# Kernel optimization log

Hardware: AMD Instinct MI355X
Metric: run time of the kernel (lower is better)

Reference implementation:

```python
import jax, jax.numpy as jnp
import numpy as np

LEAKY_SLOPE = 0.2   # LeakyReLU alpha from __init__
MASK_VAL = -9.0e15  # same sentinel as torch reference


def setup_inputs() -> dict:
    key = jax.random.key(0)
    k1, k2, k3 = jax.random.split(key, 3)
    B, N, D = 512, 64, 128
    hidden = jax.random.normal(k1, (B, N, D), dtype=jnp.float32)
    adj = jax.random.randint(k2, (B, N, N), 0, 5)  # edge types 0..4
    a = jax.random.normal(k3, (4, D), dtype=jnp.float32) * 0.1  # stacked a_0..a_3
    return {"hidden": hidden, "adj": adj, "a": a}


def reference(hidden, adj, a):
    # e_k[b,i,j] = leakyrelu( sum_d hidden[b,i,d]*hidden[b,j,d]*a[k,d] )
    # Never materializes the [B,N,N,D] tensor: contract (hidden * a_k) @ hidden^T.
    e = jnp.einsum('kd,bid,bjd->kbij', a, hidden, hidden)  # [4,B,N,N]
    e = jnp.where(e >= 0, e, LEAKY_SLOPE * e)
    mask = jnp.full(e.shape[1:], MASK_VAL, dtype=e.dtype)
    alpha = jnp.where(adj == 1, e[0], mask)
    alpha = jnp.where(adj == 2, e[1], alpha)
    alpha = jnp.where(adj == 3, e[2], alpha)
    alpha = jnp.where(adj == 4, e[3], alpha)
    alpha = jax.nn.softmax(alpha, axis=-1)          # [B,N,N]
    return jnp.matmul(alpha, hidden)                # [B,N,D]
```

## Files before the change

### kernel.cpp

```cpp
#include <hip/hip_runtime.h>
#include <hip/hip_bf16.h>


#define NB 512
#define NN 64
#define ND 128
#define HS 136
#define AS 72

typedef __bf16 bf16x8 __attribute__((ext_vector_type(8)));
typedef __bf16 bf16x4 __attribute__((ext_vector_type(4)));
typedef float  f32x4  __attribute__((ext_vector_type(4)));

__global__ __launch_bounds__(256)
void gat_kernel(const float* __restrict__ hidden,
                const int*   __restrict__ adj,
                const float* __restrict__ a,
                float*       __restrict__ out)
{
    __shared__ __bf16 h_lds[NN * HS];
    __shared__ __bf16 h_tr[8 * NN * 16];
    __shared__ __bf16 al_lds[NN * AS];
    __shared__ float  a_lds[4 * ND];

    const int t = threadIdx.x;
    const int l = t & 63;
    const int w = t >> 6;
    const int b = blockIdx.x;
    const int g  = l >> 4;
    const int g8 = g << 3;
    const int i0 = w * 16 + (g << 2);

    const int* adjb = adj + (size_t)b * NN * NN;
    int adjv[4][4];
    #pragma unroll
    for (int ct = 0; ct < 4; ++ct)
        #pragma unroll
        for (int r = 0; r < 4; ++r)
            adjv[ct][r] = adjb[(i0 + r) * NN + ct * 16 + (l & 15)];

    const float4* hin = (const float4*)(hidden + (size_t)b * NN * ND);
    #pragma unroll
    for (int it = 0; it < 8; ++it) {
        int row = ((l >> 2) & 15) | ((it >> 1) << 4);
        int f4  = (l & 3) | (w << 2) | ((it & 1) << 4);
        float4 v = hin[row * 32 + f4];
        bf16x4 pk = { (__bf16)v.x, (__bf16)v.y, (__bf16)v.z, (__bf16)v.w };
        int c4 = f4 << 2;
        *(bf16x4*)&h_lds[row * HS + c4] = pk;
        *(bf16x4*)&h_tr[((c4 >> 4) << 10) + (row << 4) + (c4 & 15)] = pk;
    }
    a_lds[t]       = a[t];
    a_lds[t + 256] = a[t + 256];
    __syncthreads();

    const int irow = w * 16 + (l & 15);
    f32x4 acc[4][4];
    #pragma unroll
    for (int ct = 0; ct < 4; ++ct)
        #pragma unroll
        for (int k = 0; k < 4; ++k)
            acc[ct][k] = (f32x4){0.f, 0.f, 0.f, 0.f};

    #pragma unroll
    for (int kk = 0; kk < 4; ++kk) {
        int d0 = kk * 32 + g8;
        bf16x8 hf = *(const bf16x8*)&h_lds[irow * HS + d0];
        float hff[8];
        #pragma unroll
        for (int e = 0; e < 8; ++e) hff[e] = (float)hf[e];
        bf16x8 hk[4];
        #pragma unroll
        for (int k = 0; k < 4; ++k) {
            float4 alo = *(const float4*)&a_lds[k * ND + d0];
            float4 ahi = *(const float4*)&a_lds[k * ND + d0 + 4];
            bf16x8 r;
            r[0] = (__bf16)(hff[0] * alo.x); r[1] = (__bf16)(hff[1] * alo.y);
            r[2] = (__bf16)(hff[2] * alo.z); r[3] = (__bf16)(hff[3] * alo.w);
            r[4] = (__bf16)(hff[4] * ahi.x); r[5] = (__bf16)(hff[5] * ahi.y);
            r[6] = (__bf16)(hff[6] * ahi.z); r[7] = (__bf16)(hff[7] * ahi.w);
            hk[k] = r;
        }
        bf16x8 bfr[4];
        #pragma unroll
        for (int ct = 0; ct < 4; ++ct)
            bfr[ct] = *(const bf16x8*)&h_lds[(ct * 16 + (l & 15)) * HS + d0];
        #pragma unroll
        for (int ct = 0; ct < 4; ++ct)
            #pragma unroll
            for (int k = 0; k < 4; ++k)
                acc[ct][k] = __builtin_amdgcn_mfma_f32_16x16x32_bf16(hk[k], bfr[ct], acc[ct][k], 0, 0, 0);
    }

    float sel[4][4];
    #pragma unroll
    for (int ct = 0; ct < 4; ++ct)
        #pragma unroll
        for (int r = 0; r < 4; ++r) {
            float e0 = fmaxf(acc[ct][0][r], 0.2f * acc[ct][0][r]);
            float e1 = fmaxf(acc[ct][1][r], 0.2f * acc[ct][1][r]);
            float e2 = fmaxf(acc[ct][2][r], 0.2f * acc[ct][2][r]);
            float e3 = fmaxf(acc[ct][3][r], 0.2f * acc[ct][3][r]);
            int av = adjv[ct][r];
            sel[ct][r] = av == 1 ? e0 : av == 2 ? e1 : av == 3 ? e2 : av == 4 ? e3 : -9.0e15f;
        }

    float inv[4];
    #pragma unroll
    for (int r = 0; r < 4; ++r) {
        float m = fmaxf(fmaxf(sel[0][r], sel[1][r]), fmaxf(sel[2][r], sel[3][r]));
        m = fmaxf(m, __shfl_xor(m, 1));
        m = fmaxf(m, __shfl_xor(m, 2));
        m = fmaxf(m, __shfl_xor(m, 4));
        m = fmaxf(m, __shfl_xor(m, 8));
        float p0 = __expf(sel[0][r] - m);
        float p1 = __expf(sel[1][r] - m);
        float p2 = __expf(sel[2][r] - m);
        float p3 = __expf(sel[3][r] - m);
        float s = p0 + p1 + p2 + p3;
        s += __shfl_xor(s, 1);
        s += __shfl_xor(s, 2);
        s += __shfl_xor(s, 4);
        s += __shfl_xor(s, 8);
        inv[r] = 1.0f / s;
        int i = i0 + r;
        al_lds[i * AS +  0 + (l & 15)] = (__bf16)p0;
        al_lds[i * AS + 16 + (l & 15)] = (__bf16)p1;
        al_lds[i * AS + 32 + (l & 15)] = (__bf16)p2;
        al_lds[i * AS + 48 + (l & 15)] = (__bf16)p3;
    }

    const int ia = w * 16 + (l & 15);
    bf16x8 aA0 = *(const bf16x8*)&al_lds[ia * AS + g8];
    bf16x8 aA1 = *(const bf16x8*)&al_lds[ia * AS + 32 + g8];
    float* outb = out + (size_t)b * NN * ND;
    unsigned trb = (unsigned)(unsigned long long)(&h_tr[0])
                 + (unsigned)(((l & 15) << 3) + (g << 8));
    #pragma unroll
    for (int dt = 0; dt < 8; ++dt) {
        unsigned ab = trb + dt * 2048;
        bf16x4 r0, r1, r2, r3;
        asm volatile("ds_read_b64_tr_b16 %0, %1"             : "=v"(r0) : "v"(ab));
        asm volatile("ds_read_b64_tr_b16 %0, %1 offset:128"  : "=v"(r1) : "v"(ab));
        asm volatile("ds_read_b64_tr_b16 %0, %1 offset:1024" : "=v"(r2) : "v"(ab));
        asm volatile("ds_read_b64_tr_b16 %0, %1 offset:1152" : "=v"(r3) : "v"(ab));
        asm volatile("s_waitcnt lgkmcnt(0)" ::: "memory");
        __builtin_amdgcn_sched_barrier(0);
        bf16x8 B0 = __builtin_shufflevector(r0, r1, 0, 1, 2, 3, 4, 5, 6, 7);
        bf16x8 B1 = __builtin_shufflevector(r2, r3, 0, 1, 2, 3, 4, 5, 6, 7);
        f32x4 o = {0.f, 0.f, 0.f, 0.f};
        o = __builtin_amdgcn_mfma_f32_16x16x32_bf16(aA0, B0, o, 0, 0, 0);
        o = __builtin_amdgcn_mfma_f32_16x16x32_bf16(aA1, B1, o, 0, 0, 0);
        int dr = dt * 16 + (l & 15);
        #pragma unroll
        for (int r = 0; r < 4; ++r)
            outb[(i0 + r) * ND + dr] = o[r] * inv[r];
    }
}

extern "C" void kernel_launch(void* const* d_in, const int* in_sizes, int n_in,
                              void* d_out, int out_size, void* d_ws, size_t ws_size,
                              hipStream_t stream) {
    const float* hidden = (const float*)d_in[0];
    const int*   adj    = (const int*)d_in[1];
    const float* a      = (const float*)d_in[2];
    float*       out    = (float*)d_out;
    gat_kernel<<<NB, 256, 0, stream>>>(hidden, adj, a, out);
}
```

Baseline: 16.62 us.

## Stage adjacency in LDS and swap MFMA operands for vectorized output stores

Adjacency is now loaded with coalesced int4 global reads into a padded LDS tile instead of 16 scattered scalar global loads per thread. The softmax normalization is folded into the bf16 probabilities before the second matmul. The MFMA operand order is swapped so each lane holds four consecutive output columns of one row, which allows float4 stores instead of scalar stores. The cost is extra LDS space (about 16KB), which may lower occupancy, plus scalar LDS writes for the adjacency tile and slight precision loss from normalizing before rounding to bf16.

New measurement: 17.12 us. 3.0% more time.

```diff
diff --git a/kernel.cpp b/kernel.cpp
--- a/kernel.cpp
+++ b/kernel.cpp
@@ -7,6 +7,7 @@
 #define ND 128
 #define HS 136
 #define AS 72
+#define AJS 65
 
 typedef __bf16 bf16x8 __attribute__((ext_vector_type(8)));
 typedef __bf16 bf16x4 __attribute__((ext_vector_type(4)));
@@ -22,6 +23,7 @@
     __shared__ __bf16 h_tr[8 * NN * 16];
     __shared__ __bf16 al_lds[NN * AS];
     __shared__ float  a_lds[4 * ND];
+    __shared__ int    adj_lds[NN * AJS];
 
     const int t = threadIdx.x;
     const int l = t & 63;
@@ -30,14 +32,6 @@
     const int g  = l >> 4;
     const int g8 = g << 3;
     const int i0 = w * 16 + (g << 2);
-
-    const int* adjb = adj + (size_t)b * NN * NN;
-    int adjv[4][4];
-    #pragma unroll
-    for (int ct = 0; ct < 4; ++ct)
-        #pragma unroll
-        for (int r = 0; r < 4; ++r)
-            adjv[ct][r] = adjb[(i0 + r) * NN + ct * 16 + (l & 15)];
 
     const float4* hin = (const float4*)(hidden + (size_t)b * NN * ND);
     #pragma unroll
@@ -49,6 +43,16 @@
         int c4 = f4 << 2;
         *(bf16x4*)&h_lds[row * HS + c4] = pk;
         *(bf16x4*)&h_tr[((c4 >> 4) << 10) + (row << 4) + (c4 & 15)] = pk;
+    }
+    const int4* adjin = (const int4*)(adj + (size_t)b * NN * NN);
+    #pragma unroll
+    for (int it = 0; it < 4; ++it) {
+        int idx = it * 256 + t;
+        int4 v = adjin[idx];
+        int ri = idx >> 4;
+        int c4 = (idx & 15) << 2;
+        int* p = &adj_lds[ri * AJS + c4];
+        p[0] = v.x; p[1] = v.y; p[2] = v.z; p[3] = v.w;
     }
     a_lds[t]       = a[t];
     a_lds[t + 256] = a[t + 256];
@@ -97,15 +101,14 @@
     for (int ct = 0; ct < 4; ++ct)
         #pragma unroll
         for (int r = 0; r < 4; ++r) {
+            int av = adj_lds[(i0 + r) * AJS + ct * 16 + (l & 15)];
             float e0 = fmaxf(acc[ct][0][r], 0.2f * acc[ct][0][r]);
             float e1 = fmaxf(acc[ct][1][r], 0.2f * acc[ct][1][r]);
             float e2 = fmaxf(acc[ct][2][r], 0.2f * acc[ct][2][r]);
             float e3 = fmaxf(acc[ct][3][r], 0.2f * acc[ct][3][r]);
-            int av = adjv[ct][r];
             sel[ct][r] = av == 1 ? e0 : av == 2 ? e1 : av == 3 ? e2 : av == 4 ? e3 : -9.0e15f;
         }
 
-    float inv[4];
     #pragma unroll
     for (int r = 0; r < 4; ++r) {
         float m = fmaxf(fmaxf(sel[0][r], sel[1][r]), fmaxf(sel[2][r], sel[3][r]));
@@ -122,17 +125,17 @@
         s += __shfl_xor(s, 2);
         s += __shfl_xor(s, 4);
         s += __shfl_xor(s, 8);
-        inv[r] = 1.0f / s;
+        float inv = 1.0f / s;
         int i = i0 + r;
-        al_lds[i * AS +  0 + (l & 15)] = (__bf16)p0;
-        al_lds[i * AS + 16 + (l & 15)] = (__bf16)p1;
-        al_lds[i * AS + 32 + (l & 15)] = (__bf16)p2;
-        al_lds[i * AS + 48 + (l & 15)] = (__bf16)p3;
+        al_lds[i * AS +  0 + (l & 15)] = (__bf16)(p0 * inv);
+        al_lds[i * AS + 16 + (l & 15)] = (__bf16)(p1 * inv);
+        al_lds[i * AS + 32 + (l & 15)] = (__bf16)(p2 * inv);
+        al_lds[i * AS + 48 + (l & 15)] = (__bf16)(p3 * inv);
     }
 
     const int ia = w * 16 + (l & 15);
-    bf16x8 aA0 = *(const bf16x8*)&al_lds[ia * AS + g8];
-    bf16x8 aA1 = *(const bf16x8*)&al_lds[ia * AS + 32 + g8];
+    bf16x8 pB0 = *(const bf16x8*)&al_lds[ia * AS + g8];
+    bf16x8 pB1 = *(const bf16x8*)&al_lds[ia * AS + 32 + g8];
     float* outb = out + (size_t)b * NN * ND;
     unsigned trb = (unsigned)(unsigned long long)(&h_tr[0])
                  + (unsigned)(((l & 15) << 3) + (g << 8));
@@ -146,15 +149,13 @@
         asm volatile("ds_read_b64_tr_b16 %0, %1 offset:1152" : "=v"(r3) : "v"(ab));
         asm volatile("s_waitcnt lgkmcnt(0)" ::: "memory");
         __builtin_amdgcn_sched_barrier(0);
-        bf16x8 B0 = __builtin_shufflevector(r0, r1, 0, 1, 2, 3, 4, 5, 6, 7);
-        bf16x8 B1 = __builtin_shufflevector(r2, r3, 0, 1, 2, 3, 4, 5, 6, 7);
+        bf16x8 A0 = __builtin_shufflevector(r0, r1, 0, 1, 2, 3, 4, 5, 6, 7);
+        bf16x8 A1 = __builtin_shufflevector(r2, r3, 0, 1, 2, 3, 4, 5, 6, 7);
         f32x4 o = {0.f, 0.f, 0.f, 0.f};
-        o = __builtin_amdgcn_mfma_f32_16x16x32_bf16(aA0, B0, o, 0, 0, 0);
-        o = __builtin_amdgcn_mfma_f32_16x16x32_bf16(aA1, B1, o, 0, 0, 0);
-        int dr = dt * 16 + (l & 15);
-        #pragma unroll
-        for (int r = 0; r < 4; ++r)
-            outb[(i0 + r) * ND + dr] = o[r] * inv[r];
+        o = __builtin_amdgcn_mfma_f32_16x16x32_bf16(A0, pB0, o, 0, 0, 0);
+        o = __builtin_amdgcn_mfma_f32_16x16x32_bf16(A1, pB1, o, 0, 0, 0);
+        float4 st = { o[0], o[1], o[2], o[3] };
+        *(float4*)&outb[ia * ND + dt * 16 + (g << 2)] = st;
     }
 }
 
```

## Split each batch across two blocks by row halves with transposed coalesced output stores

Applied to the files above, without the earlier changes.

Launches two blocks per batch, each handling 32 of the 64 query rows, so the grid has 1024 blocks instead of 512. Only two waves compute scores and softmax, and all four waves then share the output GEMM. The operands are swapped so each lane writes a float4 of consecutive output columns, giving coalesced stores. Each block still loads and converts the whole hidden tile, so global reads of hidden double, and half the waves sit idle during the score phase.

Result: slower. 21.15 us (+27.3%).

```diff
diff --git a/kernel.cpp b/kernel.cpp
--- a/kernel.cpp
+++ b/kernel.cpp
@@ -2,7 +2,6 @@
 #include <hip/hip_bf16.h>
 
 
-#define NB 512
 #define NN 64
 #define ND 128
 #define HS 136
@@ -12,7 +11,7 @@
 typedef __bf16 bf16x4 __attribute__((ext_vector_type(4)));
 typedef float  f32x4  __attribute__((ext_vector_type(4)));
 
-__global__ __launch_bounds__(256)
+__global__ __launch_bounds__(256, 3)
 void gat_kernel(const float* __restrict__ hidden,
                 const int*   __restrict__ adj,
                 const float* __restrict__ a,
@@ -20,30 +19,35 @@
 {
     __shared__ __bf16 h_lds[NN * HS];
     __shared__ __bf16 h_tr[8 * NN * 16];
-    __shared__ __bf16 al_lds[NN * AS];
+    __shared__ __bf16 al_lds[32 * AS];
     __shared__ float  a_lds[4 * ND];
+    __shared__ float  inv_lds[32];
 
-    const int t = threadIdx.x;
-    const int l = t & 63;
-    const int w = t >> 6;
-    const int b = blockIdx.x;
+    const int t   = threadIdx.x;
+    const int l   = t & 63;
+    const int w   = t >> 6;
+    const int bid = blockIdx.x;
+    const int b    = ((bid >> 4) << 3) | (bid & 7);
+    const int half = (bid >> 3) & 1;
     const int g  = l >> 4;
     const int g8 = g << 3;
-    const int i0 = w * 16 + (g << 2);
 
     const int* adjb = adj + (size_t)b * NN * NN;
     int adjv[4][4];
-    #pragma unroll
-    for (int ct = 0; ct < 4; ++ct)
+    if (w < 2) {
+        const int i0 = half * 32 + w * 16 + (g << 2);
         #pragma unroll
-        for (int r = 0; r < 4; ++r)
-            adjv[ct][r] = adjb[(i0 + r) * NN + ct * 16 + (l & 15)];
+        for (int ct = 0; ct < 4; ++ct)
+            #pragma unroll
+            for (int r = 0; r < 4; ++r)
+                adjv[ct][r] = adjb[(i0 + r) * NN + ct * 16 + (l & 15)];
+    }
 
     const float4* hin = (const float4*)(hidden + (size_t)b * NN * ND);
     #pragma unroll
-    for (int it = 0; it < 8; ++it) {
-        int row = ((l >> 2) & 15) | ((it >> 1) << 4);
-        int f4  = (l & 3) | (w << 2) | ((it & 1) << 4);
+    for (int s = 0; s < 8; ++s) {
+        int row = ((l >> 2) & 15) | ((s >> 1) << 4);
+        int f4  = (l & 3) | (w << 2) | ((s & 1) << 4);
         float4 v = hin[row * 32 + f4];
         bf16x4 pk = { (__bf16)v.x, (__bf16)v.y, (__bf16)v.z, (__bf16)v.w };
         int c4 = f4 << 2;
@@ -54,90 +58,96 @@
     a_lds[t + 256] = a[t + 256];
     __syncthreads();
 
-    const int irow = w * 16 + (l & 15);
-    f32x4 acc[4][4];
-    #pragma unroll
-    for (int ct = 0; ct < 4; ++ct)
-        #pragma unroll
-        for (int k = 0; k < 4; ++k)
-            acc[ct][k] = (f32x4){0.f, 0.f, 0.f, 0.f};
-
-    #pragma unroll
-    for (int kk = 0; kk < 4; ++kk) {
-        int d0 = kk * 32 + g8;
-        bf16x8 hf = *(const bf16x8*)&h_lds[irow * HS + d0];
-        float hff[8];
-        #pragma unroll
-        for (int e = 0; e < 8; ++e) hff[e] = (float)hf[e];
-        bf16x8 hk[4];
-        #pragma unroll
-        for (int k = 0; k < 4; ++k) {
-            float4 alo = *(const float4*)&a_lds[k * ND + d0];
-            float4 ahi = *(const float4*)&a_lds[k * ND + d0 + 4];
-            bf16x8 r;
-            r[0] = (__bf16)(hff[0] * alo.x); r[1] = (__bf16)(hff[1] * alo.y);
-            r[2] = (__bf16)(hff[2] * alo.z); r[3] = (__bf16)(hff[3] * alo.w);
-            r[4] = (__bf16)(hff[4] * ahi.x); r[5] = (__bf16)(hff[5] * ahi.y);
-            r[6] = (__bf16)(hff[6] * ahi.z); r[7] = (__bf16)(hff[7] * ahi.w);
-            hk[k] = r;
-        }
-        bf16x8 bfr[4];
-        #pragma unroll
-        for (int ct = 0; ct < 4; ++ct)
-            bfr[ct] = *(const bf16x8*)&h_lds[(ct * 16 + (l & 15)) * HS + d0];
+    if (w < 2) {
+        const int i0   = half * 32 + w * 16 + (g << 2);
+        const int irow = half * 32 + w * 16 + (l & 15);
+        f32x4 acc[4][4];
         #pragma unroll
         for (int ct = 0; ct < 4; ++ct)
             #pragma unroll
             for (int k = 0; k < 4; ++k)
-                acc[ct][k] = __builtin_amdgcn_mfma_f32_16x16x32_bf16(hk[k], bfr[ct], acc[ct][k], 0, 0, 0);
-    }
+                acc[ct][k] = (f32x4){0.f, 0.f, 0.f, 0.f};
 
-    float sel[4][4];
-    #pragma unroll
-    for (int ct = 0; ct < 4; ++ct)
+        #pragma unroll
+        for (int kk = 0; kk < 4; ++kk) {
+            int d0 = kk * 32 + g8;
+            bf16x8 hf = *(const bf16x8*)&h_lds[irow * HS + d0];
+            float hff[8];
+            #pragma unroll
+            for (int e = 0; e < 8; ++e) hff[e] = (float)hf[e];
+            bf16x8 hk[4];
+            #pragma unroll
+            for (int k = 0; k < 4; ++k) {
+                float4 alo = *(const float4*)&a_lds[k * ND + d0];
+                float4 ahi = *(const float4*)&a_lds[k * ND + d0 + 4];
+                bf16x8 r;
+                r[0] = (__bf16)(hff[0] * alo.x); r[1] = (__bf16)(hff[1] * alo.y);
+                r[2] = (__bf16)(hff[2] * alo.z); r[3] = (__bf16)(hff[3] * alo.w);
+                r[4] = (__bf16)(hff[4] * ahi.x); r[5] = (__bf16)(hff[5] * ahi.y);
+                r[6] = (__bf16)(hff[6] * ahi.z); r[7] = (__bf16)(hff[7] * ahi.w);
+                hk[k] = r;
+            }
+            bf16x8 bfr[4];
+            #pragma unroll
+            for (int ct = 0; ct < 4; ++ct)
+                bfr[ct] = *(const bf16x8*)&h_lds[(ct * 16 + (l & 15)) * HS + d0];
+            #pragma unroll
+            for (int ct = 0; ct < 4; ++ct)
+                #pragma unroll
+                for (int k = 0; k < 4; ++k)
+                    acc[ct][k] = __builtin_amdgcn_mfma_f32_16x16x32_bf16(hk[k], bfr[ct], acc[ct][k], 0, 0, 0);
+        }
+
+        float sel[4][4];
+        #pragma unroll
+        for (int ct = 0; ct < 4; ++ct)
+            #pragma unroll
+            for (int r = 0; r < 4; ++r) {
+                int av = adjv[ct][r];
+                float e0 = fmaxf(acc[ct][0][r], 0.2f * acc[ct][0][r]);
+                float e1 = fmaxf(acc[ct][1][r], 0.2f * acc[ct][1][r]);
+                float e2 = fmaxf(acc[ct][2][r], 0.2f * acc[ct][2][r]);
+                float e3 = fmaxf(acc[ct][3][r], 0.2f * acc[ct][3][r]);
+                sel[ct][r] = av == 1 ? e0 : av == 2 ? e1 : av == 3 ? e2 : av == 4 ? e3 : -9.0e15f;
+            }
+
         #pragma unroll
         for (int r = 0; r < 4; ++r) {
-            float e0 = fmaxf(acc[ct][0][r], 0.2f * acc[ct][0][r]);
-            float e1 = fmaxf(acc[ct][1][r], 0.2f * acc[ct][1][r]);
-            float e2 = fmaxf(acc[ct][2][r], 0.2f * acc[ct][2][r]);
-            float e3 = fmaxf(acc[ct][3][r], 0.2f * acc[ct][3][r]);
-            int av = adjv[ct][r];
-            sel[ct][r] = av == 1 ? e0 : av == 2 ? e1 : av == 3 ? e2 : av == 4 ? e3 : -9.0e15f;
+            float m = fmaxf(fmaxf(sel[0][r], sel[1][r]), fmaxf(sel[2][r], sel[3][r]));
+            m = fmaxf(m, __shfl_xor(m, 1));
+            m = fmaxf(m, __shfl_xor(m, 2));
+            m = fmaxf(m, __shfl_xor(m, 4));
+            m = fmaxf(m, __shfl_xor(m, 8));
+            float p0 = __expf(sel[0][r] - m);
+            float p1 = __expf(sel[1][r] - m);
+            float p2 = __expf(sel[2][r] - m);
+            float p3 = __expf(sel[3][r] - m);
+            float s = p0 + p1 + p2 + p3;
+            s += __shfl_xor(s, 1);
+            s += __shfl_xor(s, 2);
+            s += __shfl_xor(s, 4);
+            s += __shfl_xor(s, 8);
+            int lr = w * 16 + (g << 2) + r;
+            al_lds[lr * AS +  0 + (l & 15)] = (__bf16)p0;
+            al_lds[lr * AS + 16 + (l & 15)] = (__bf16)p1;
+            al_lds[lr * AS + 32 + (l & 15)] = (__bf16)p2;
+            al_lds[lr * AS + 48 + (l & 15)] = (__bf16)p3;
+            if ((l & 15) == 0) inv_lds[lr] = 1.0f / s;
         }
+    }
+    __syncthreads();
 
-    float inv[4];
-    #pragma unroll
-    for (int r = 0; r < 4; ++r) {
-        float m = fmaxf(fmaxf(sel[0][r], sel[1][r]), fmaxf(sel[2][r], sel[3][r]));
-        m = fmaxf(m, __shfl_xor(m, 1));
-        m = fmaxf(m, __shfl_xor(m, 2));
-        m = fmaxf(m, __shfl_xor(m, 4));
-        m = fmaxf(m, __shfl_xor(m, 8));
-        float p0 = __expf(sel[0][r] - m);
-        float p1 = __expf(sel[1][r] - m);
-        float p2 = __expf(sel[2][r] - m);
-        float p3 = __expf(sel[3][r] - m);
-        float s = p0 + p1 + p2 + p3;
-        s += __shfl_xor(s, 1);
-        s += __shfl_xor(s, 2);
-        s += __shfl_xor(s, 4);
-        s += __shfl_xor(s, 8);
-        inv[r] = 1.0f / s;
-        int i = i0 + r;
-        al_lds[i * AS +  0 + (l & 15)] = (__bf16)p0;
-        al_lds[i * AS + 16 + (l & 15)] = (__bf16)p1;
-        al_lds[i * AS + 32 + (l & 15)] = (__bf16)p2;
-        al_lds[i * AS + 48 + (l & 15)] = (__bf16)p3;
-    }
-
-    const int ia = w * 16 + (l & 15);
-    bf16x8 aA0 = *(const bf16x8*)&al_lds[ia * AS + g8];
-    bf16x8 aA1 = *(const bf16x8*)&al_lds[ia * AS + 32 + g8];
+    const int it2 = w & 1;
+    const int lr  = it2 * 16 + (l & 15);
+    bf16x8 pB0 = *(const bf16x8*)&al_lds[lr * AS + g8];
+    bf16x8 pB1 = *(const bf16x8*)&al_lds[lr * AS + 32 + g8];
+    float invr = inv_lds[lr];
     float* outb = out + (size_t)b * NN * ND;
     unsigned trb = (unsigned)(unsigned long long)(&h_tr[0])
                  + (unsigned)(((l & 15) << 3) + (g << 8));
     #pragma unroll
-    for (int dt = 0; dt < 8; ++dt) {
+    for (int q = 0; q < 4; ++q) {
+        int dt = (w >> 1) * 4 + q;
         unsigned ab = trb + dt * 2048;
         bf16x4 r0, r1, r2, r3;
         asm volatile("ds_read_b64_tr_b16 %0, %1"             : "=v"(r0) : "v"(ab));
@@ -146,15 +156,13 @@
         asm volatile("ds_read_b64_tr_b16 %0, %1 offset:1152" : "=v"(r3) : "v"(ab));
         asm volatile("s_waitcnt lgkmcnt(0)" ::: "memory");
         __builtin_amdgcn_sched_barrier(0);
-        bf16x8 B0 = __builtin_shufflevector(r0, r1, 0, 1, 2, 3, 4, 5, 6, 7);
-        bf16x8 B1 = __builtin_shufflevector(r2, r3, 0, 1, 2, 3, 4, 5, 6, 7);
+        bf16x8 A0 = __builtin_shufflevector(r0, r1, 0, 1, 2, 3, 4, 5, 6, 7);
+        bf16x8 A1 = __builtin_shufflevector(r2, r3, 0, 1, 2, 3, 4, 5, 6, 7);
         f32x4 o = {0.f, 0.f, 0.f, 0.f};
-        o = __builtin_amdgcn_mfma_f32_16x16x32_bf16(aA0, B0, o, 0, 0, 0);
-        o = __builtin_amdgcn_mfma_f32_16x16x32_bf16(aA1, B1, o, 0, 0, 0);
-        int dr = dt * 16 + (l & 15);
-        #pragma unroll
-        for (int r = 0; r < 4; ++r)
-            outb[(i0 + r) * ND + dr] = o[r] * inv[r];
+        o = __builtin_amdgcn_mfma_f32_16x16x32_bf16(A0, pB0, o, 0, 0, 0);
+        o = __builtin_amdgcn_mfma_f32_16x16x32_bf16(A1, pB1, o, 0, 0, 0);
+        float4 st = { o[0] * invr, o[1] * invr, o[2] * invr, o[3] * invr };
+        *(float4*)&outb[(half * 32 + lr) * ND + dt * 16 + (g << 2)] = st;
     }
 }
 
@@ -165,5 +173,5 @@
     const int*   adj    = (const int*)d_in[1];
     const float* a      = (const float*)d_in[2];
     float*       out    = (float*)d_out;
-    gat_kernel<<<NB, 256, 0, stream>>>(hidden, adj, a, out);
+    gat_kernel<<<1024, 256, 0, stream>>>(hidden, adj, a, out);
 }
```
